# Performance work log

Hardware: AMD Instinct MI355X
Metric: run time of the kernel (lower is better)

The kernel has to match this reference:

```python
import jax, jax.numpy as jnp
import numpy as np

B, S, D, H, Dh = 2, 1024, 2048, 16, 128
EPS = 1e-6


def setup_inputs() -> dict:
    key = jax.random.key(0)
    ks = jax.random.split(key, 8)
    hidden_states = jax.random.normal(ks[0], (B, S, D), jnp.float32)
    def qweight(k):
        return jax.random.randint(k, (D, D), -127, 128, dtype=jnp.int32)
    wq, wk, wv, wo = qweight(ks[1]), qweight(ks[2]), qweight(ks[3]), qweight(ks[4])
    def scale(k):
        # per-output-channel dequant scale ~ O(1/(127*sqrt(D)))
        return jax.random.uniform(k, (D,), jnp.float32, 0.5, 1.5) / (127.0 * np.sqrt(D))
    wq_s, wk_s, wv_s, wo_s = scale(ks[5]), scale(ks[6]), scale(ks[7]), scale(jax.random.fold_in(key, 99))
    qn_w = jnp.ones((D,), jnp.float32)
    kn_w = jnp.ones((D,), jnp.float32)
    # RoPE tables (rotate-half convention): [S, Dh]
    pos = jnp.arange(S, dtype=jnp.float32)
    inv_freq = 1.0 / (10000.0 ** (jnp.arange(0, Dh, 2, dtype=jnp.float32) / Dh))
    freqs = pos[:, None] * inv_freq[None, :]              # [S, Dh/2]
    cos = jnp.concatenate([jnp.cos(freqs)] * 2, axis=-1)  # [S, Dh]
    sin = jnp.concatenate([jnp.sin(freqs)] * 2, axis=-1)
    lengths = jnp.array([S, 3 * S // 4], dtype=jnp.int32)
    return dict(hidden_states=hidden_states, wq_s=wq_s, wk_s=wk_s, wv_s=wv_s,
                wo_s=wo_s, qn_w=qn_w, kn_w=kn_w, cos=cos, sin=sin,
                wq=wq, wk=wk, wv=wv, wo=wo, lengths=lengths)


def _q8_linear(x, w_int, scale):
    # Q8Linear: int8 weight [out,in] dequantized by per-output-channel scale
    w = w_int.astype(jnp.float32) * scale[:, None]
    return jnp.einsum('bsd,od->bso', x, w)


def _rms_norm(x, w):
    var = jnp.mean(jnp.square(x), axis=-1, keepdims=True)
    return x * jax.lax.rsqrt(var + EPS) * w


def _apply_rope(x, cos, sin):
    # x: [B,S,D] -> per-head rotate-half RoPE -> [B,S,D]
    xh = x.reshape(B, S, H, Dh)
    x1, x2 = jnp.split(xh, 2, axis=-1)
    rot = jnp.concatenate([-x2, x1], axis=-1)
    out = xh * cos[None, :, None, :] + rot * sin[None, :, None, :]
    return out.reshape(B, S, D)


def reference(hidden_states, wq_s, wk_s, wv_s, wo_s, qn_w, kn_w, cos, sin,
              wq, wk, wv, wo, lengths):
    q = _rms_norm(_q8_linear(hidden_states, wq, wq_s), qn_w)
    k = _rms_norm(_q8_linear(hidden_states, wk, wk_s), kn_w)
    v = _q8_linear(hidden_states, wv, wv_s)
    q = _apply_rope(q, cos, sin)
    k = _apply_rope(k, cos, sin)
    # [B,S,D] -> [B,H,S,Dh]
    q = q.reshape(B, S, H, Dh).transpose(0, 2, 1, 3)
    k = k.reshape(B, S, H, Dh).transpose(0, 2, 1, 3)
    v = v.reshape(B, S, H, Dh).transpose(0, 2, 1, 3)
    # length mask -> additive bias [B,1,1,S]
    positions = jnp.arange(S)
    valid = positions[None, :] < lengths[:, None]
    bias = jnp.where(valid, 0.0, -jnp.inf).astype(jnp.float32)[:, None, None, :]
    scores = jnp.einsum('bhqd,bhkd->bhqk', q, k) / np.sqrt(Dh) + bias
    probs = jax.nn.softmax(scores, axis=-1)
    attn = jnp.einsum('bhqk,bhkd->bhqd', probs, v)
    attn = attn.transpose(0, 2, 1, 3).reshape(B, S, D)
    out = _q8_linear(attn, wo, wo_s)
    return out
```

## Files before the change

### kernel.cpp

```cpp
#include <hip/hip_runtime.h>
#include <stdint.h>

typedef __bf16 bf16;
typedef bf16 bf16x8 __attribute__((ext_vector_type(8)));
typedef bf16 bf16x4 __attribute__((ext_vector_type(4)));
typedef float f32x4 __attribute__((ext_vector_type(4)));

#define B_   2
#define S_   1024
#define D_   2048
#define H_   16
#define DH_  128
#define M_   (B_*S_)
#define EPSF 1e-6f

__device__ __forceinline__ void gload_lds16(const void* g, void* l) {
    __builtin_amdgcn_global_load_lds(
        (const __attribute__((address_space(1))) void*)g,
        (__attribute__((address_space(3))) void*)l,
        16, 0, 0);
}

struct ConvArgs {
    const void* s[4];
    bf16* d[4];
};

__global__ __launch_bounds__(256) void conv_all(ConvArgs a, int n) {
    const int z = blockIdx.y;
    const int i = (blockIdx.x * 256 + threadIdx.x) * 8;
    if (i + 8 > n) return;
    bf16x8 o;
    if (z == 0) {
        const float* src = (const float*)a.s[0];
        float4 v0 = *(const float4*)(src + i);
        float4 v1 = *(const float4*)(src + i + 4);
        o[0] = (bf16)v0.x; o[1] = (bf16)v0.y; o[2] = (bf16)v0.z; o[3] = (bf16)v0.w;
        o[4] = (bf16)v1.x; o[5] = (bf16)v1.y; o[6] = (bf16)v1.z; o[7] = (bf16)v1.w;
    } else {
        const int* src = (const int*)a.s[z];
        int4 v0 = *(const int4*)(src + i);
        int4 v1 = *(const int4*)(src + i + 4);
        o[0] = (bf16)(float)v0.x; o[1] = (bf16)(float)v0.y;
        o[2] = (bf16)(float)v0.z; o[3] = (bf16)(float)v0.w;
        o[4] = (bf16)(float)v1.x; o[5] = (bf16)(float)v1.y;
        o[6] = (bf16)(float)v1.z; o[7] = (bf16)(float)v1.w;
    }
    *(bf16x8*)(a.d[z] + i) = o;
}

struct GemmArgs {
    const bf16* W[3];
    const float* Sc[3];
    void* O[3];
    int mode[3];
    const int* wo_src;
    bf16* wo_dst;
};

__global__ __launch_bounds__(512, 2) void gemm8p(const bf16* __restrict__ A, GemmArgs args) {
    __shared__ char lds[131072];
    constexpr int NT = D_ / 64;
    const int z = blockIdx.z;
    const int t = threadIdx.x;

    if (z == 3) {
        const int flat = blockIdx.y * 8 + blockIdx.x;
        const int* src = args.wo_src + (size_t)flat * 65536;
        bf16* dst = args.wo_dst + (size_t)flat * 65536;
#pragma unroll
        for (int it = 0; it < 16; ++it) {
            int off = it * 4096 + t * 8;
            int4 v0 = *(const int4*)(src + off);
            int4 v1 = *(const int4*)(src + off + 4);
            bf16x8 o;
            o[0] = (bf16)(float)v0.x; o[1] = (bf16)(float)v0.y;
            o[2] = (bf16)(float)v0.z; o[3] = (bf16)(float)v0.w;
            o[4] = (bf16)(float)v1.x; o[5] = (bf16)(float)v1.y;
            o[6] = (bf16)(float)v1.z; o[7] = (bf16)(float)v1.w;
            *(bf16x8*)(dst + off) = o;
        }
        return;
    }

    const bf16* __restrict__ Wz = args.W[z];
    const float* __restrict__ Sc = args.Sc[z];
    const int mode = args.mode[z];
    const int w = t >> 6, l = t & 63;
    const int wr = w >> 2, wc = w & 3;
    const int m0 = blockIdx.y * 256, n0 = blockIdx.x * 256;
    const int hi = l >> 4, lo = l & 15;

    const int r8 = l >> 3;
    const int ce = ((l & 7) ^ (r8 & 7)) * 8;
    const bf16* Ag = A  + (size_t)(m0 + w * 8 + r8) * D_ + ce;
    const bf16* Bg = Wz + (size_t)(n0 + w * 8 + r8) * D_ + ce;

    auto stage = [&](int kt, int q) {
        if (kt >= NT) return;
        const bf16* g = (q < 2 ? Ag : Bg) + (size_t)((q & 1) * 128) * D_ + (size_t)kt * 64;
        char* d = lds + ((kt & 1) ? 65536 : 0) + q * 16384 + w * 1024;
        gload_lds16((const void*)g, (void*)d);
        gload_lds16((const void*)(g + (size_t)64 * D_), (void*)(d + 8192));
    };

    f32x4 acc[8][4] = {};

    stage(0, 0); stage(0, 1); stage(0, 2); stage(0, 3);
    stage(1, 2); stage(1, 0);
    asm volatile("s_waitcnt vmcnt(4)" ::: "memory");
    asm volatile("s_barrier" ::: "memory");

    for (int kt = 0; kt < NT; ++kt) {
        const char* Pb = lds + ((kt & 1) ? 65536 : 0);
        const char* As = Pb;
        const char* Bs = Pb + 32768;
        bf16x8 a[4][2], b01[2][2], b23[2][2];

        auto rdA = [&](int mi, int kk) -> bf16x8 {
            int row = wr * 128 + mi * 16 + lo;
            return *(const bf16x8*)(As + row * 128 + ((kk * 64 + hi * 16) ^ ((row & 7) << 4)));
        };
        auto rdB = [&](int ni, int kk) -> bf16x8 {
            int row = wc * 64 + ni * 16 + lo;
            return *(const bf16x8*)(Bs + row * 128 + ((kk * 64 + hi * 16) ^ ((row & 7) << 4)));
        };

#pragma unroll
        for (int mi = 0; mi < 4; ++mi) { a[mi][0] = rdA(mi, 0); a[mi][1] = rdA(mi, 1); }
#pragma unroll
        for (int ni = 0; ni < 2; ++ni) { b01[ni][0] = rdB(ni, 0); b01[ni][1] = rdB(ni, 1); }
        stage(kt + 1, 1);
        asm volatile("s_barrier" ::: "memory");
        asm volatile("s_waitcnt lgkmcnt(0)" ::: "memory");
        __builtin_amdgcn_sched_barrier(0);
        __builtin_amdgcn_s_setprio(1);
#pragma unroll
        for (int mi = 0; mi < 4; ++mi)
#pragma unroll
            for (int ni = 0; ni < 2; ++ni)
#pragma unroll
                for (int kk = 0; kk < 2; ++kk)
                    acc[mi][ni] = __builtin_amdgcn_mfma_f32_16x16x32_bf16(a[mi][kk], b01[ni][kk], acc[mi][ni], 0, 0, 0);
        __builtin_amdgcn_s_setprio(0);
        asm volatile("s_barrier" ::: "memory");

#pragma unroll
        for (int ni = 0; ni < 2; ++ni) { b23[ni][0] = rdB(2 + ni, 0); b23[ni][1] = rdB(2 + ni, 1); }
        stage(kt + 1, 3);
        asm volatile("s_barrier" ::: "memory");
        asm volatile("s_waitcnt lgkmcnt(0)" ::: "memory");
        __builtin_amdgcn_sched_barrier(0);
        __builtin_amdgcn_s_setprio(1);
#pragma unroll
        for (int mi = 0; mi < 4; ++mi)
#pragma unroll
            for (int ni = 0; ni < 2; ++ni)
#pragma unroll
                for (int kk = 0; kk < 2; ++kk)
                    acc[mi][2 + ni] = __builtin_amdgcn_mfma_f32_16x16x32_bf16(a[mi][kk], b23[ni][kk], acc[mi][2 + ni], 0, 0, 0);
        __builtin_amdgcn_s_setprio(0);
        asm volatile("s_barrier" ::: "memory");

#pragma unroll
        for (int mi = 0; mi < 4; ++mi) { a[mi][0] = rdA(4 + mi, 0); a[mi][1] = rdA(4 + mi, 1); }
        stage(kt + 2, 2);
        asm volatile("s_barrier" ::: "memory");
        asm volatile("s_waitcnt lgkmcnt(0)" ::: "memory");
        __builtin_amdgcn_sched_barrier(0);
        __builtin_amdgcn_s_setprio(1);
#pragma unroll
        for (int mi = 0; mi < 4; ++mi)
#pragma unroll
            for (int ni = 0; ni < 2; ++ni)
#pragma unroll
                for (int kk = 0; kk < 2; ++kk)
                    acc[4 + mi][2 + ni] = __builtin_amdgcn_mfma_f32_16x16x32_bf16(a[mi][kk], b23[ni][kk], acc[4 + mi][2 + ni], 0, 0, 0);
        __builtin_amdgcn_s_setprio(0);
        asm volatile("s_barrier" ::: "memory");

        stage(kt + 2, 0);
        asm volatile("s_barrier" ::: "memory");
        __builtin_amdgcn_sched_barrier(0);
        __builtin_amdgcn_s_setprio(1);
#pragma unroll
        for (int mi = 0; mi < 4; ++mi)
#pragma unroll
            for (int ni = 0; ni < 2; ++ni)
#pragma unroll
                for (int kk = 0; kk < 2; ++kk)
                    acc[4 + mi][ni] = __builtin_amdgcn_mfma_f32_16x16x32_bf16(a[mi][kk], b01[ni][kk], acc[4 + mi][ni], 0, 0, 0);
        __builtin_amdgcn_s_setprio(0);
        if (kt < NT - 2) asm volatile("s_waitcnt vmcnt(4)" ::: "memory");
        else             asm volatile("s_waitcnt vmcnt(0)" ::: "memory");
        asm volatile("s_barrier" ::: "memory");
    }

#pragma unroll
    for (int ni = 0; ni < 4; ++ni) {
        const int n = n0 + wc * 64 + ni * 16 + lo;
        const float scv = Sc[n];
#pragma unroll
        for (int mi = 0; mi < 8; ++mi) {
            const int mb = m0 + wr * 128 + mi * 16 + hi * 4;
            if (mode == 1) {
                bf16x4 pk;
#pragma unroll
                for (int r = 0; r < 4; ++r) pk[r] = (bf16)(acc[mi][ni][r] * scv);
                const int bb = mb >> 10, s = mb & 1023, hh = n >> 7, dh = n & 127;
                *(bf16x4*)(((bf16*)args.O[z]) + (((size_t)(bb * H_ + hh)) * DH_ + dh) * S_ + s) = pk;
            } else {
#pragma unroll
                for (int r = 0; r < 4; ++r)
                    ((bf16*)args.O[z])[(size_t)(mb + r) * D_ + n] = (bf16)(acc[mi][ni][r] * scv);
            }
        }
    }
}

__global__ __launch_bounds__(256, 2) void gemmO(const bf16* __restrict__ A, const bf16* __restrict__ W,
                                                const float* __restrict__ Sc, float* __restrict__ O) {
    __shared__ char lds[65536];
    constexpr int NT = D_ / 64;
    const int t = threadIdx.x;
    const int w = t >> 6, l = t & 63;
    const int wr = w >> 1, wc = w & 1;
    const int m0 = blockIdx.y * 128, n0 = blockIdx.x * 128;
    const int hi = l >> 4, lo = l & 15;

    const int r8 = l >> 3;
    const int ce = ((l & 7) ^ (r8 & 7)) * 8;
    const bf16* Ag = A + (size_t)(m0 + w * 8 + r8) * D_ + ce;
    const bf16* Bg = W + (size_t)(n0 + w * 8 + r8) * D_ + ce;

    auto stage = [&](int kt) {
        char* d = lds + (kt & 1) * 32768 + w * 1024;
        const bf16* ga = Ag + (size_t)kt * 64;
        const bf16* gb = Bg + (size_t)kt * 64;
#pragma unroll
        for (int j = 0; j < 4; ++j) {
            gload_lds16((const void*)(ga + (size_t)j * 32 * D_), (void*)(d + j * 4096));
            gload_lds16((const void*)(gb + (size_t)j * 32 * D_), (void*)(d + 16384 + j * 4096));
        }
    };

    f32x4 acc[4][4] = {};
    stage(0);
    for (int kt = 0; kt < NT; ++kt) {
        const char* cur = lds + (kt & 1) * 32768;
        if (kt + 1 < NT) {
            stage(kt + 1);
            asm volatile("s_waitcnt vmcnt(8)" ::: "memory");
        } else {
            asm volatile("s_waitcnt vmcnt(0)" ::: "memory");
        }
        asm volatile("s_barrier" ::: "memory");

        bf16x8 a[4][2], b[4][2];
#pragma unroll
        for (int mi = 0; mi < 4; ++mi)
#pragma unroll
            for (int kk = 0; kk < 2; ++kk) {
                int row = wr * 64 + mi * 16 + lo;
                a[mi][kk] = *(const bf16x8*)(cur + row * 128 + ((kk * 64 + hi * 16) ^ ((row & 7) << 4)));
            }
#pragma unroll
        for (int ni = 0; ni < 4; ++ni)
#pragma unroll
            for (int kk = 0; kk < 2; ++kk) {
                int row = wc * 64 + ni * 16 + lo;
                b[ni][kk] = *(const bf16x8*)(cur + 16384 + row * 128 + ((kk * 64 + hi * 16) ^ ((row & 7) << 4)));
            }
        __builtin_amdgcn_s_setprio(1);
#pragma unroll
        for (int mi = 0; mi < 4; ++mi)
#pragma unroll
            for (int ni = 0; ni < 4; ++ni)
#pragma unroll
                for (int kk = 0; kk < 2; ++kk)
                    acc[mi][ni] = __builtin_amdgcn_mfma_f32_16x16x32_bf16(a[mi][kk], b[ni][kk], acc[mi][ni], 0, 0, 0);
        __builtin_amdgcn_s_setprio(0);
        asm volatile("s_barrier" ::: "memory");
    }

#pragma unroll
    for (int ni = 0; ni < 4; ++ni) {
        const int n = n0 + wc * 64 + ni * 16 + lo;
        const float scv = Sc[n];
#pragma unroll
        for (int mi = 0; mi < 4; ++mi) {
            const int mb = m0 + wr * 64 + mi * 16 + hi * 4;
#pragma unroll
            for (int r = 0; r < 4; ++r)
                O[(size_t)(mb + r) * D_ + n] = acc[mi][ni][r] * scv;
        }
    }
}

__global__ __launch_bounds__(256) void rope_norm(const bf16* __restrict__ qr, const bf16* __restrict__ kr,
                                                 const float* __restrict__ qn, const float* __restrict__ kn,
                                                 const float* __restrict__ cosT, const float* __restrict__ sinT,
                                                 bf16* __restrict__ qOut, bf16* __restrict__ kOut) {
    const int which = blockIdx.z;
    const bf16* src = which ? kr : qr;
    const float* nw = which ? kn : qn;
    bf16* dst = which ? kOut : qOut;
    const int row = blockIdx.x;
    const int b = row >> 10, s = row & 1023;
    const int t = threadIdx.x;
    __shared__ float xs[D_];
    __shared__ float red[4];

    bf16x8 v = *(const bf16x8*)(src + (size_t)row * D_ + t * 8);
    float x[8]; float ss = 0.f;
#pragma unroll
    for (int j = 0; j < 8; ++j) { x[j] = (float)v[j]; ss += x[j] * x[j]; xs[t * 8 + j] = x[j]; }
#pragma unroll
    for (int msk = 32; msk; msk >>= 1) ss += __shfl_xor(ss, msk, 64);
    if ((t & 63) == 0) red[t >> 6] = ss;
    __syncthreads();
    const float inv = rsqrtf((red[0] + red[1] + red[2] + red[3]) / (float)D_ + EPSF);

    const int h = t >> 4;
    const int dh0 = (t & 15) * 8;
    bf16x8 o;
#pragma unroll
    for (int j = 0; j < 8; ++j) {
        int dd = dh0 + j;
        int d = h * 128 + dd;
        int pd = (dd < 64) ? d + 64 : d - 64;
        float xn = x[j] * inv * nw[d];
        float xp = xs[pd] * inv * nw[pd];
        float rot = (dd < 64) ? -xp : xp;
        o[j] = (bf16)(xn * cosT[s * DH_ + dd] + rot * sinT[s * DH_ + dd]);
    }
    *(bf16x8*)(dst + (((size_t)(b * H_ + h)) * S_ + s) * DH_ + dh0) = o;
}

__global__ __launch_bounds__(512) void flash(const bf16* __restrict__ Q, const bf16* __restrict__ Kb,
                                             const bf16* __restrict__ VTb, const int* __restrict__ lengths,
                                             bf16* __restrict__ Out) {
    __shared__ bf16 Qs[128 * 128];
    __shared__ bf16 Ks[64 * 128];
    __shared__ bf16 Vt[128 * 64];
    __shared__ bf16 Ps[8][16 * 64];
    const int t = threadIdx.x, w = t >> 6, l = t & 63;
    const int bh = blockIdx.y;
    const int b = bh >> 4;
    const int q0 = blockIdx.x * 128;
    const int L = lengths[b];
    const size_t base = (size_t)bh * S_ * DH_;
    const size_t vbase = (size_t)bh * DH_ * S_;
    const int hi = l >> 4, lo = l & 15;
    const int swz = (lo & 7) << 3;

    {
        const bf16* src = Q + base + (size_t)q0 * DH_;
#pragma unroll
        for (int i = 0; i < 4; ++i) {
            int pb = w * 4 + i;
            int r = pb * 4 + (l >> 4);
            int sb = ((l & 15) * 16) ^ ((r & 7) << 4);
            gload_lds16((const void*)(src + (size_t)r * DH_ + (sb >> 1)), (void*)(Qs + pb * 512));
        }
    }

    f32x4 O[8] = {};
    float mrow[4], lrow[4];
#pragma unroll
    for (int r = 0; r < 4; ++r) { mrow[r] = -1e30f; lrow[r] = 0.f; }
    const int nt = (L + 63) >> 6;
    const float sscale = 0.08838834764831843f;

    for (int kt = 0; kt < nt; ++kt) {
        const int k0 = kt * 64;
        __syncthreads();
        {
            const bf16* ksrc = Kb + base + (size_t)k0 * DH_;
#pragma unroll
            for (int i = 0; i < 2; ++i) {
                int pb = w * 2 + i;
                int r = pb * 4 + (l >> 4);
                int sb = ((l & 15) * 16) ^ ((r & 7) << 4);
                gload_lds16((const void*)(ksrc + (size_t)r * DH_ + (sb >> 1)), (void*)(Ks + pb * 512));
            }
        }
        {
            const bf16* vsrc = VTb + vbase + k0;
#pragma unroll
            for (int i = 0; i < 2; ++i) {
                int pb = w * 2 + i;
                int d = pb * 8 + (l >> 3);
                int sb = ((l & 7) * 16) ^ ((d & 7) << 4);
                gload_lds16((const void*)(vsrc + (size_t)d * S_ + (sb >> 1)), (void*)(Vt + pb * 512));
            }
        }
        __syncthreads();

        f32x4 sc[4] = {};
        __builtin_amdgcn_s_setprio(1);
#pragma unroll
        for (int kk = 0; kk < 4; ++kk) {
            const int ko = kk * 32 + hi * 8;
            bf16x8 aq = *(const bf16x8*)(Qs + (w * 16 + lo) * 128 + (ko ^ swz));
#pragma unroll
            for (int ni = 0; ni < 4; ++ni) {
                bf16x8 bk = *(const bf16x8*)(Ks + (ni * 16 + lo) * 128 + (ko ^ swz));
                sc[ni] = __builtin_amdgcn_mfma_f32_16x16x32_bf16(aq, bk, sc[ni], 0, 0, 0);
            }
        }
        __builtin_amdgcn_s_setprio(0);

        float p[4][4];
#pragma unroll
        for (int r = 0; r < 4; ++r) {
            float sv[4]; float vmax = -1e30f;
#pragma unroll
            for (int ni = 0; ni < 4; ++ni) {
                int kg = k0 + ni * 16 + lo;
                float vv = sc[ni][r] * sscale;
                if (kg >= L) vv = -1e30f;
                sv[ni] = vv;
                vmax = fmaxf(vmax, vv);
            }
#pragma unroll
            for (int msk = 1; msk < 16; msk <<= 1) vmax = fmaxf(vmax, __shfl_xor(vmax, msk, 64));
            float mnew = fmaxf(mrow[r], vmax);
            float corr = __expf(mrow[r] - mnew);
            float rs = 0.f;
#pragma unroll
            for (int ni = 0; ni < 4; ++ni) { float pv = __expf(sv[ni] - mnew); p[r][ni] = pv; rs += pv; }
#pragma unroll
            for (int msk = 1; msk < 16; msk <<= 1) rs += __shfl_xor(rs, msk, 64);
            lrow[r] = lrow[r] * corr + rs;
            mrow[r] = mnew;
#pragma unroll
            for (int di = 0; di < 8; ++di) O[di][r] *= corr;
        }

#pragma unroll
        for (int r = 0; r < 4; ++r) {
            int prow = hi * 4 + r;
#pragma unroll
            for (int ni = 0; ni < 4; ++ni)
                Ps[w][prow * 64 + (((ni * 16 + lo)) ^ ((prow & 7) << 3))] = (bf16)p[r][ni];
        }

        __builtin_amdgcn_s_setprio(1);
#pragma unroll
        for (int kk = 0; kk < 2; ++kk) {
            const int ko = kk * 32 + hi * 8;
            bf16x8 ap = *(const bf16x8*)(&Ps[w][lo * 64 + (ko ^ swz)]);
#pragma unroll
            for (int di = 0; di < 8; ++di) {
                bf16x8 bv = *(const bf16x8*)(Vt + (di * 16 + lo) * 64 + (ko ^ swz));
                O[di] = __builtin_amdgcn_mfma_f32_16x16x32_bf16(ap, bv, O[di], 0, 0, 0);
            }
        }
        __builtin_amdgcn_s_setprio(0);
    }

    const int h = bh & 15;
#pragma unroll
    for (int r = 0; r < 4; ++r) {
        float invl = 1.0f / lrow[r];
        int qrow = q0 + w * 16 + hi * 4 + r;
        bf16* orow = Out + (size_t)(b * S_ + qrow) * D_ + h * DH_;
#pragma unroll
        for (int di = 0; di < 8; ++di)
            orow[di * 16 + lo] = (bf16)(O[di][r] * invl);
    }
}

extern "C" void kernel_launch(void* const* d_in, const int* in_sizes, int n_in,
                              void* d_out, int out_size, void* d_ws, size_t ws_size,
                              hipStream_t stream) {
    const float* x    = (const float*)d_in[0];
    const float* wq_s = (const float*)d_in[1];
    const float* wk_s = (const float*)d_in[2];
    const float* wv_s = (const float*)d_in[3];
    const float* wo_s = (const float*)d_in[4];
    const float* qn   = (const float*)d_in[5];
    const float* kn   = (const float*)d_in[6];
    const float* cosT = (const float*)d_in[7];
    const float* sinT = (const float*)d_in[8];
    const int* wq = (const int*)d_in[9];
    const int* wk = (const int*)d_in[10];
    const int* wv = (const int*)d_in[11];
    const int* wo = (const int*)d_in[12];
    const int* lengths = (const int*)d_in[13];
    float* out = (float*)d_out;

    char* ws = (char*)d_ws;
    const size_t SLOT = (size_t)M_ * D_ * sizeof(bf16);
    bf16* xb   = (bf16*)(ws);
    bf16* wqb  = (bf16*)(ws + 1 * SLOT);
    bf16* wkb  = (bf16*)(ws + 2 * SLOT);
    bf16* wvb  = (bf16*)(ws + 3 * SLOT);
    bf16* wob  = (bf16*)(ws + 4 * SLOT);
    bf16* qr   = (bf16*)(ws + 5 * SLOT);
    bf16* kr   = (bf16*)(ws + 6 * SLOT);
    bf16* qb2  = (bf16*)(ws + 7 * SLOT);
    bf16* kb2  = (bf16*)(ws + 8 * SLOT);
    bf16* vb2  = (bf16*)(ws + 9 * SLOT);
    bf16* attnb = qr;

    const int NW = D_ * D_;
    ConvArgs ca;
    ca.s[0] = x;  ca.d[0] = xb;
    ca.s[1] = wq; ca.d[1] = wqb;
    ca.s[2] = wk; ca.d[2] = wkb;
    ca.s[3] = wv; ca.d[3] = wvb;
    conv_all<<<dim3(NW / 2048, 4), dim3(256), 0, stream>>>(ca, NW);

    GemmArgs ga;
    ga.W[0] = wqb; ga.W[1] = wkb; ga.W[2] = wvb;
    ga.Sc[0] = wq_s; ga.Sc[1] = wk_s; ga.Sc[2] = wv_s;
    ga.O[0] = qr; ga.O[1] = kr; ga.O[2] = vb2;
    ga.mode[0] = 2; ga.mode[1] = 2; ga.mode[2] = 1;
    ga.wo_src = wo; ga.wo_dst = wob;
    gemm8p<<<dim3(D_ / 256, M_ / 256, 4), dim3(512), 0, stream>>>(xb, ga);

    rope_norm<<<dim3(M_, 1, 2), dim3(256), 0, stream>>>(qr, kr, qn, kn, cosT, sinT, qb2, kb2);

    flash<<<dim3(S_ / 128, B_ * H_, 1), dim3(512), 0, stream>>>(qb2, kb2, vb2, lengths, attnb);

    gemmO<<<dim3(D_ / 128, M_ / 128), dim3(256), 0, stream>>>(attnb, wob, wo_s, out);
}
```

Baseline: 161.5 us.

## Prefetch next K/V tile into registers and halve flash query tile

Shrinks the flash-attention block from 128 to 64 query rows (256 threads, twice the blocks) and replaces the synchronous per-tile global-to-LDS K/V load with a register prefetch of the next tile. That prefetch overlaps with the QK and PV MFMA work and is written to swizzled LDS after a barrier. The aim is to hide global load latency and raise occupancy and parallelism. In exchange it adds register pressure from the prefetch buffers, reloads K/V once per 64-row query block instead of per 128 rows, and relies on hand-placed waitcnt and barriers.

Result: slower. 199.5 us (+23.5%).

```diff
diff --git a/kernel.cpp b/kernel.cpp
--- a/kernel.cpp
+++ b/kernel.cpp
@@ -337,17 +337,17 @@
     *(bf16x8*)(dst + (((size_t)(b * H_ + h)) * S_ + s) * DH_ + dh0) = o;
 }
 
-__global__ __launch_bounds__(512) void flash(const bf16* __restrict__ Q, const bf16* __restrict__ Kb,
+__global__ __launch_bounds__(256) void flash(const bf16* __restrict__ Q, const bf16* __restrict__ Kb,
                                              const bf16* __restrict__ VTb, const int* __restrict__ lengths,
                                              bf16* __restrict__ Out) {
-    __shared__ bf16 Qs[128 * 128];
+    __shared__ bf16 Qs[64 * 128];
     __shared__ bf16 Ks[64 * 128];
     __shared__ bf16 Vt[128 * 64];
-    __shared__ bf16 Ps[8][16 * 64];
+    __shared__ bf16 Ps[4][16 * 64];
     const int t = threadIdx.x, w = t >> 6, l = t & 63;
     const int bh = blockIdx.y;
     const int b = bh >> 4;
-    const int q0 = blockIdx.x * 128;
+    const int q0 = blockIdx.x * 64;
     const int L = lengths[b];
     const size_t base = (size_t)bh * S_ * DH_;
     const size_t vbase = (size_t)bh * DH_ * S_;
@@ -355,15 +355,22 @@
     const int swz = (lo & 7) << 3;
 
     {
-        const bf16* src = Q + base + (size_t)q0 * DH_;
+        const bf16* qsrc = Q + base + (size_t)q0 * DH_;
+        const bf16* ksrc = Kb + base;
+        const bf16* vsrc = VTb + vbase;
 #pragma unroll
         for (int i = 0; i < 4; ++i) {
-            int pb = w * 4 + i;
-            int r = pb * 4 + (l >> 4);
-            int sb = ((l & 15) * 16) ^ ((r & 7) << 4);
-            gload_lds16((const void*)(src + (size_t)r * DH_ + (sb >> 1)), (void*)(Qs + pb * 512));
-        }
-    }
+            int r = (w * 4 + i) * 4 + hi;
+            int sb = (lo * 16) ^ ((r & 7) << 4);
+            gload_lds16((const void*)((const char*)(qsrc + (size_t)r * DH_) + sb), (void*)(Qs + (w * 4 + i) * 512));
+            gload_lds16((const void*)((const char*)(ksrc + (size_t)r * DH_) + sb), (void*)(Ks + (w * 4 + i) * 512));
+            int d = (w * 4 + i) * 8 + (l >> 3);
+            int sbv = ((l & 7) * 16) ^ ((d & 7) << 4);
+            gload_lds16((const void*)((const char*)(vsrc + (size_t)d * S_) + sbv), (void*)(Vt + (w * 4 + i) * 512));
+        }
+    }
+    asm volatile("s_waitcnt vmcnt(0)" ::: "memory");
+    asm volatile("s_barrier" ::: "memory");
 
     f32x4 O[8] = {};
     float mrow[4], lrow[4];
@@ -374,28 +381,19 @@
 
     for (int kt = 0; kt < nt; ++kt) {
         const int k0 = kt * 64;
-        __syncthreads();
-        {
-            const bf16* ksrc = Kb + base + (size_t)k0 * DH_;
-#pragma unroll
-            for (int i = 0; i < 2; ++i) {
-                int pb = w * 2 + i;
-                int r = pb * 4 + (l >> 4);
-                int sb = ((l & 15) * 16) ^ ((r & 7) << 4);
-                gload_lds16((const void*)(ksrc + (size_t)r * DH_ + (sb >> 1)), (void*)(Ks + pb * 512));
-            }
-        }
-        {
-            const bf16* vsrc = VTb + vbase + k0;
-#pragma unroll
-            for (int i = 0; i < 2; ++i) {
-                int pb = w * 2 + i;
-                int d = pb * 8 + (l >> 3);
-                int sb = ((l & 7) * 16) ^ ((d & 7) << 4);
-                gload_lds16((const void*)(vsrc + (size_t)d * S_ + (sb >> 1)), (void*)(Vt + pb * 512));
-            }
-        }
-        __syncthreads();
+        int4 kreg[4], vreg[4];
+        const bool pre = (kt + 1 < nt);
+        if (pre) {
+            const char* knx = (const char*)(Kb + base + (size_t)(k0 + 64) * DH_);
+            const char* vnx = (const char*)(VTb + vbase + (k0 + 64));
+#pragma unroll
+            for (int j = 0; j < 4; ++j) {
+                int g = t + 256 * j;
+                kreg[j] = *(const int4*)(knx + (g >> 4) * 256 + (g & 15) * 16);
+                vreg[j] = *(const int4*)(vnx + (size_t)(g >> 3) * (S_ * 2) + (g & 7) * 16);
+            }
+            __builtin_amdgcn_sched_barrier(0);
+        }
 
         f32x4 sc[4] = {};
         __builtin_amdgcn_s_setprio(1);
@@ -458,6 +456,20 @@
             }
         }
         __builtin_amdgcn_s_setprio(0);
+
+        asm volatile("s_barrier" ::: "memory");
+        if (pre) {
+#pragma unroll
+            for (int j = 0; j < 4; ++j) {
+                int g = t + 256 * j;
+                int r = g >> 4, cb = (g & 15) * 16;
+                *(int4*)((char*)Ks + r * 256 + (cb ^ ((r & 7) << 4))) = kreg[j];
+                int d = g >> 3, cbv = (g & 7) * 16;
+                *(int4*)((char*)Vt + d * 128 + (cbv ^ ((d & 7) << 4))) = vreg[j];
+            }
+            asm volatile("s_waitcnt lgkmcnt(0)" ::: "memory");
+        }
+        asm volatile("s_barrier" ::: "memory");
     }
 
     const int h = bh & 15;
@@ -523,7 +535,7 @@
 
     rope_norm<<<dim3(M_, 1, 2), dim3(256), 0, stream>>>(qr, kr, qn, kn, cosT, sinT, qb2, kb2);
 
-    flash<<<dim3(S_ / 128, B_ * H_, 1), dim3(512), 0, stream>>>(qb2, kb2, vb2, lengths, attnb);
+    flash<<<dim3(S_ / 64, B_ * H_, 1), dim3(256), 0, stream>>>(qb2, kb2, vb2, lengths, attnb);
 
     gemmO<<<dim3(D_ / 128, M_ / 128), dim3(256), 0, stream>>>(attnb, wob, wo_s, out);
 }
```
